# Kernel tuning notes

Hardware: AMD Instinct MI355X
Metric: run time of the kernel (lower is better)

The kernel has to match this reference:

```python
import jax, jax.numpy as jnp
import numpy as np

HEAD_DIM = 64


def setup_inputs() -> dict:
    key = jax.random.key(0)
    ks = jax.random.split(key, 5)
    B, T, D = 2, 2048, 1024
    x = jax.random.normal(ks[0], (B, T, D), dtype=jnp.float32)
    # Linear weights stored as [in, out]; scaled like typical init.
    w_qkv = jax.random.normal(ks[1], (D, 3 * D), dtype=jnp.float32) / np.sqrt(D)
    b_qkv = jax.random.normal(ks[2], (3 * D,), dtype=jnp.float32) * 0.02
    w_o = jax.random.normal(ks[3], (D, D), dtype=jnp.float32) / np.sqrt(D)
    b_o = jax.random.normal(ks[4], (D,), dtype=jnp.float32) * 0.02
    return {"x": x, "w_qkv": w_qkv, "b_qkv": b_qkv, "w_o": w_o, "b_o": b_o,
            "window": 256}


def reference(x, w_qkv, b_qkv, w_o, b_o, window):
    B, T, D = x.shape
    H = D // HEAD_DIM
    qkv = x @ w_qkv + b_qkv                      # [B, T, 3D]
    q, k, v = jnp.split(qkv, 3, axis=-1)
    # [B, H, T, hd]
    q = q.reshape(B, T, H, HEAD_DIM).transpose(0, 2, 1, 3)
    k = k.reshape(B, T, H, HEAD_DIM).transpose(0, 2, 1, 3)
    v = v.reshape(B, T, H, HEAD_DIM).transpose(0, 2, 1, 3)
    # Causal band mask: key j valid for query i iff 0 <= i - j <= window.
    idx = jnp.arange(T)
    diff = idx[:, None] - idx[None, :]
    mask = (diff >= 0) & (diff <= window)        # [T, T] bool
    scale = 1.0 / np.sqrt(HEAD_DIM)
    scores = jnp.einsum("bhqd,bhkd->bhqk", q, k) * scale
    scores = jnp.where(mask, scores, -jnp.inf)
    attn = jax.nn.softmax(scores, axis=-1)       # each row has >=1 valid entry
    out = jnp.einsum("bhqk,bhkd->bhqd", attn, v)  # [B, H, T, hd]
    out = out.transpose(0, 2, 1, 3).reshape(B, T, D)
    return out @ w_o + b_o
```

## Files before the change

### kernel.cpp

```cpp
#include <hip/hip_runtime.h>

#define T_SEQ 2048
#define DMODEL 1024
#define NH 16
#define HD 64

typedef unsigned short u16;
typedef short s16;
typedef __attribute__((ext_vector_type(8))) unsigned short u16x8;
typedef __attribute__((ext_vector_type(4))) unsigned short u16x4;
typedef __attribute__((ext_vector_type(8))) short bf16x8;
typedef __attribute__((ext_vector_type(4))) float f32x4;

__device__ __forceinline__ u16 f2bf(float f) {
    union { float f; unsigned u; } v; v.f = f;
    unsigned r = v.u + 0x7fffu + ((v.u >> 16) & 1u);
    return (u16)(r >> 16);
}
__device__ __forceinline__ float bf2f(u16 u) {
    union { unsigned u; float f; } v; v.u = ((unsigned)u) << 16;
    return v.f;
}

__device__ __forceinline__ void gl_lds16(const u16* g, u16* l) {
    __builtin_amdgcn_global_load_lds(
        (const __attribute__((address_space(1))) unsigned int*)g,
        (__attribute__((address_space(3))) unsigned int*)l, 16, 0, 0);
}

__global__ __launch_bounds__(256) void convert_kernel(
    const float* __restrict__ in, u16* __restrict__ out, int n)
{
    int idx = (blockIdx.x * 256 + threadIdx.x) * 4;
    if (idx < n) {
        float4 v = *reinterpret_cast<const float4*>(&in[idx]);
        u16x4 o;
        o.x = f2bf(v.x); o.y = f2bf(v.y); o.z = f2bf(v.z); o.w = f2bf(v.w);
        *reinterpret_cast<u16x4*>(&out[idx]) = o;
    }
}

__global__ __launch_bounds__(256) void transpose_convert_kernel(
    const float* __restrict__ in, u16* __restrict__ out, int K, int N)
{
    __shared__ u16 tile[64][65];
    const int tid = threadIdx.x;
    const int k0 = blockIdx.y * 64, n0 = blockIdx.x * 64;
    const int r  = tid >> 2;
    const int c4 = (tid & 3) * 16;
    #pragma unroll
    for (int i = 0; i < 4; ++i) {
        float4 v = *reinterpret_cast<const float4*>(&in[(size_t)(k0 + r) * N + n0 + c4 + i * 4]);
        tile[c4 + i*4 + 0][r] = f2bf(v.x);
        tile[c4 + i*4 + 1][r] = f2bf(v.y);
        tile[c4 + i*4 + 2][r] = f2bf(v.z);
        tile[c4 + i*4 + 3][r] = f2bf(v.w);
    }
    __syncthreads();
    u16x8 o0, o1;
    #pragma unroll
    for (int i = 0; i < 8; ++i) o0[i] = tile[r][c4 + i];
    #pragma unroll
    for (int i = 0; i < 8; ++i) o1[i] = tile[r][c4 + 8 + i];
    *reinterpret_cast<u16x8*>(&out[(size_t)(n0 + r) * K + k0 + c4])     = o0;
    *reinterpret_cast<u16x8*>(&out[(size_t)(n0 + r) * K + k0 + c4 + 8]) = o1;
}

template<int BM, int BN, bool OUT_BF16>
__global__ __launch_bounds__(256) void gemm_mfma_kernel(
    const u16* __restrict__ A, const u16* __restrict__ BT,
    const float* __restrict__ bias,
    float* __restrict__ C, u16* __restrict__ Cb,
    int M, int N, int K)
{
    constexpr int BK = 32;
    __shared__ __align__(16) u16 As[BM * BK];
    __shared__ __align__(16) u16 Bs[BN * BK];

    const int tid  = threadIdx.x;
    const int wave = tid >> 6, lane = tid & 63;
    const int m0 = blockIdx.y * BM, n0 = blockIdx.x * BN;

    constexpr int WM = BM / 2, WN = BN / 2;
    constexpr int MF = WM / 16, NF = WN / 16;
    const int wm = (wave >> 1) * WM, wn = (wave & 1) * WN;
    const int l15 = lane & 15, l4 = lane >> 4;

    f32x4 acc[MF][NF];
    #pragma unroll
    for (int nf = 0; nf < NF; ++nf) {
        const float bv = bias[n0 + wn + nf * 16 + l15];
        #pragma unroll
        for (int mf = 0; mf < MF; ++mf)
            acc[mf][nf] = (f32x4){bv, bv, bv, bv};
    }

    const int srow = tid >> 2;
    const int soff = (tid & 3) * 8;

    for (int k0 = 0; k0 < K; k0 += BK) {
        __syncthreads();
        gl_lds16(&A[(size_t)(m0 + srow) * K + k0 + soff],       &As[(size_t)tid * 8]);
        gl_lds16(&A[(size_t)(m0 + 64 + srow) * K + k0 + soff],  &As[(size_t)(tid + 256) * 8]);
        gl_lds16(&BT[(size_t)(n0 + srow) * K + k0 + soff],      &Bs[(size_t)tid * 8]);
        if constexpr (BN == 128)
            gl_lds16(&BT[(size_t)(n0 + 64 + srow) * K + k0 + soff], &Bs[(size_t)(tid + 256) * 8]);
        __syncthreads();

        bf16x8 af[MF], bf[NF];
        #pragma unroll
        for (int mf = 0; mf < MF; ++mf)
            af[mf] = *reinterpret_cast<const bf16x8*>(&As[(wm + mf * 16 + l15) * BK + l4 * 8]);
        #pragma unroll
        for (int nf = 0; nf < NF; ++nf)
            bf[nf] = *reinterpret_cast<const bf16x8*>(&Bs[(wn + nf * 16 + l15) * BK + l4 * 8]);
        #pragma unroll
        for (int mf = 0; mf < MF; ++mf)
            #pragma unroll
            for (int nf = 0; nf < NF; ++nf)
                acc[mf][nf] = __builtin_amdgcn_mfma_f32_16x16x32_bf16(af[mf], bf[nf], acc[mf][nf], 0, 0, 0);
    }

    #pragma unroll
    for (int mf = 0; mf < MF; ++mf)
        #pragma unroll
        for (int nf = 0; nf < NF; ++nf) {
            const int col = n0 + wn + nf * 16 + l15;
            #pragma unroll
            for (int r = 0; r < 4; ++r) {
                const int row = m0 + wm + mf * 16 + l4 * 4 + r;
                if constexpr (OUT_BF16) Cb[(size_t)row * N + col] = f2bf(acc[mf][nf][r]);
                else                    C [(size_t)row * N + col] = acc[mf][nf][r];
            }
        }
}

__global__ __launch_bounds__(256) void swa_mfma_kernel(
    const u16* __restrict__ qkv, u16* __restrict__ out,
    const int* __restrict__ wptr)
{
    const int window = *wptr;
    const int qt = blockIdx.x;
    const int bh = blockIdx.y;
    const int b  = bh >> 4;
    const int h  = bh & (NH - 1);

    const int tid  = threadIdx.x;
    const int wave = tid >> 6, lane = tid & 63;
    const int l15  = lane & 15, l4 = lane >> 4;
    const int hoff = h * HD;

    __shared__ __align__(16) s16 Ks[64 * 64];
    __shared__ __align__(16) s16 Vt[64 * 64];
    __shared__ __align__(16) s16 Ps[64 * 64];

    auto swz = [](int row, int col) { return (row * 64 + col) ^ ((row & 7) << 3); };

    const size_t qgrow = (size_t)(b * T_SEQ + qt * 64 + wave * 16 + l15) * (3 * DMODEL) + hoff;
    const bf16x8 qf0 = *reinterpret_cast<const bf16x8*>(&qkv[qgrow + l4 * 8]);
    const bf16x8 qf1 = *reinterpret_cast<const bf16x8*>(&qkv[qgrow + 32 + l4 * 8]);

    f32x4 oacc[4];
    #pragma unroll
    for (int nf = 0; nf < 4; ++nf) oacc[nf] = (f32x4){0.f, 0.f, 0.f, 0.f};
    float m[4] = {-1e30f, -1e30f, -1e30f, -1e30f};
    float l[4] = {0.f, 0.f, 0.f, 0.f};

    const int lo = qt * 64 - window;
    const int cstart = (lo <= 0) ? 0 : (lo >> 6);

    const int kr = tid >> 3;
    const int kc = (tid & 7) * 8;

    for (int c = cstart; c <= qt; ++c) {
        const int j0 = c * 64;
        __syncthreads();
        #pragma unroll
        for (int pass = 0; pass < 2; ++pass) {
            const int row = kr + pass * 32;
            const size_t g = (size_t)(b * T_SEQ + j0 + row) * (3 * DMODEL) + hoff + kc;
            const bf16x8 kv8 = *reinterpret_cast<const bf16x8*>(&qkv[g + DMODEL]);
            const bf16x8 vv8 = *reinterpret_cast<const bf16x8*>(&qkv[g + 2 * DMODEL]);
            *reinterpret_cast<bf16x8*>(&Ks[swz(row, kc)]) = kv8;
            #pragma unroll
            for (int i = 0; i < 8; ++i)
                Vt[swz(kc + i, row)] = vv8[i];
        }
        __syncthreads();

        f32x4 sacc[4];
        #pragma unroll
        for (int nf = 0; nf < 4; ++nf) sacc[nf] = (f32x4){0.f, 0.f, 0.f, 0.f};
        #pragma unroll
        for (int nf = 0; nf < 4; ++nf) {
            const bf16x8 kf0 = *reinterpret_cast<const bf16x8*>(&Ks[swz(nf * 16 + l15, l4 * 8)]);
            const bf16x8 kf1 = *reinterpret_cast<const bf16x8*>(&Ks[swz(nf * 16 + l15, 32 + l4 * 8)]);
            sacc[nf] = __builtin_amdgcn_mfma_f32_16x16x32_bf16(qf0, kf0, sacc[nf], 0, 0, 0);
            sacc[nf] = __builtin_amdgcn_mfma_f32_16x16x32_bf16(qf1, kf1, sacc[nf], 0, 0, 0);
        }

        float p[4][4];
        #pragma unroll
        for (int r = 0; r < 4; ++r) {
            const int iq = qt * 64 + wave * 16 + l4 * 4 + r;
            float rmax = -1e30f;
            #pragma unroll
            for (int nf = 0; nf < 4; ++nf) {
                const int diff = iq - (j0 + nf * 16 + l15);
                const bool valid = (diff >= 0) && (diff <= window);
                const float s = valid ? sacc[nf][r] * 0.125f : -1e30f;
                p[r][nf] = s;
                rmax = fmaxf(rmax, s);
            }
            rmax = fmaxf(rmax, __shfl_xor(rmax, 1));
            rmax = fmaxf(rmax, __shfl_xor(rmax, 2));
            rmax = fmaxf(rmax, __shfl_xor(rmax, 4));
            rmax = fmaxf(rmax, __shfl_xor(rmax, 8));
            const float mn = fmaxf(m[r], rmax);
            const float rf = __expf(m[r] - mn);
            float rs = 0.f;
            #pragma unroll
            for (int nf = 0; nf < 4; ++nf) {
                const float e = __expf(p[r][nf] - mn);
                p[r][nf] = e;
                rs += e;
            }
            rs += __shfl_xor(rs, 1);
            rs += __shfl_xor(rs, 2);
            rs += __shfl_xor(rs, 4);
            rs += __shfl_xor(rs, 8);
            l[r] = l[r] * rf + rs;
            m[r] = mn;
            #pragma unroll
            for (int nf = 0; nf < 4; ++nf) oacc[nf][r] *= rf;
            #pragma unroll
            for (int nf = 0; nf < 4; ++nf)
                Ps[swz(wave * 16 + l4 * 4 + r, nf * 16 + l15)] = (s16)f2bf(p[r][nf]);
        }
        __syncthreads();

        #pragma unroll
        for (int ks = 0; ks < 2; ++ks) {
            const bf16x8 pa = *reinterpret_cast<const bf16x8*>(&Ps[swz(wave * 16 + l15, ks * 32 + l4 * 8)]);
            #pragma unroll
            for (int nf = 0; nf < 4; ++nf) {
                const bf16x8 vf = *reinterpret_cast<const bf16x8*>(&Vt[swz(nf * 16 + l15, ks * 32 + l4 * 8)]);
                oacc[nf] = __builtin_amdgcn_mfma_f32_16x16x32_bf16(pa, vf, oacc[nf], 0, 0, 0);
            }
        }
    }

    #pragma unroll
    for (int r = 0; r < 4; ++r) {
        const float inv = 1.f / l[r];
        const size_t orow = (size_t)(b * T_SEQ + qt * 64 + wave * 16 + l4 * 4 + r) * DMODEL + hoff;
        #pragma unroll
        for (int nf = 0; nf < 4; ++nf)
            out[orow + nf * 16 + l15] = f2bf(oacc[nf][r] * inv);
    }
}

extern "C" void kernel_launch(void* const* d_in, const int* in_sizes, int n_in,
                              void* d_out, int out_size, void* d_ws, size_t ws_size,
                              hipStream_t stream) {
    (void)in_sizes; (void)n_in; (void)out_size; (void)ws_size;

    const float* x     = (const float*)d_in[0];
    const float* w_qkv = (const float*)d_in[1];
    const float* b_qkv = (const float*)d_in[2];
    const float* w_o   = (const float*)d_in[3];
    const float* b_o   = (const float*)d_in[4];
    const int*   wnd   = (const int*)d_in[5];

    const int M = 2 * T_SEQ;

    char* w = (char*)d_ws;
    u16* qkvb  = (u16*)(w);
    u16* attb  = (u16*)(w + 24u * 1024 * 1024);
    u16* xb    = (u16*)(w + 32u * 1024 * 1024);
    u16* wqkvT = (u16*)(w + 40u * 1024 * 1024);
    u16* woT   = (u16*)(w + 46u * 1024 * 1024);

    dim3 blk(256);

    convert_kernel<<<dim3((M * DMODEL / 4 + 255) / 256), blk, 0, stream>>>(x, xb, M * DMODEL);
    transpose_convert_kernel<<<dim3(3 * DMODEL / 64, DMODEL / 64), blk, 0, stream>>>(
        w_qkv, wqkvT, DMODEL, 3 * DMODEL);
    transpose_convert_kernel<<<dim3(DMODEL / 64, DMODEL / 64), blk, 0, stream>>>(
        w_o, woT, DMODEL, DMODEL);

    gemm_mfma_kernel<128, 128, true><<<dim3(3 * DMODEL / 128, M / 128), blk, 0, stream>>>(
        xb, wqkvT, b_qkv, nullptr, qkvb, M, 3 * DMODEL, DMODEL);

    swa_mfma_kernel<<<dim3(T_SEQ / 64, 2 * NH), blk, 0, stream>>>(qkvb, attb, wnd);

    gemm_mfma_kernel<128, 64, false><<<dim3(DMODEL / 64, M / 128), blk, 0, stream>>>(
        attb, woT, b_o, (float*)d_out, nullptr, M, DMODEL, DMODEL);
}
```

Baseline: 176.6 us.

## Double GEMM K-tile to 64 with XOR-swizzled LDS and fix V-transpose bank conflicts

The GEMM K tile grows from 32 to 64, which halves the number of barrier-separated load/compute iterations. Global-to-LDS loads are placed with an XOR swizzle on the 8-element column chunk so the fragment reads avoid bank conflicts. The attention kernel's transposed V buffer gets a new swizzle function so the scalar transposed writes and the vector reads conflict less. The cost is doubled LDS per GEMM block, which can lower occupancy, and more fragment registers.

New measurement: 165.3 us. -6.4%, faster.

```diff
diff --git a/kernel.cpp b/kernel.cpp
--- a/kernel.cpp
+++ b/kernel.cpp
@@ -16,10 +16,6 @@
     union { float f; unsigned u; } v; v.f = f;
     unsigned r = v.u + 0x7fffu + ((v.u >> 16) & 1u);
     return (u16)(r >> 16);
-}
-__device__ __forceinline__ float bf2f(u16 u) {
-    union { unsigned u; float f; } v; v.u = ((unsigned)u) << 16;
-    return v.f;
 }
 
 __device__ __forceinline__ void gl_lds16(const u16* g, u16* l) {
@@ -73,7 +69,7 @@
     float* __restrict__ C, u16* __restrict__ Cb,
     int M, int N, int K)
 {
-    constexpr int BK = 32;
+    constexpr int BK = 64;
     __shared__ __align__(16) u16 As[BM * BK];
     __shared__ __align__(16) u16 Bs[BN * BK];
 
@@ -85,6 +81,7 @@
     constexpr int MF = WM / 16, NF = WN / 16;
     const int wm = (wave >> 1) * WM, wn = (wave & 1) * WN;
     const int l15 = lane & 15, l4 = lane >> 4;
+    const int l7  = l15 & 7;
 
     f32x4 acc[MF][NF];
     #pragma unroll
@@ -95,30 +92,47 @@
             acc[mf][nf] = (f32x4){bv, bv, bv, bv};
     }
 
-    const int srow = tid >> 2;
-    const int soff = (tid & 3) * 8;
+    constexpr int ALOADS = BM / 32;
+    constexpr int BLOADS = BN / 32;
 
     for (int k0 = 0; k0 < K; k0 += BK) {
         __syncthreads();
-        gl_lds16(&A[(size_t)(m0 + srow) * K + k0 + soff],       &As[(size_t)tid * 8]);
-        gl_lds16(&A[(size_t)(m0 + 64 + srow) * K + k0 + soff],  &As[(size_t)(tid + 256) * 8]);
-        gl_lds16(&BT[(size_t)(n0 + srow) * K + k0 + soff],      &Bs[(size_t)tid * 8]);
-        if constexpr (BN == 128)
-            gl_lds16(&BT[(size_t)(n0 + 64 + srow) * K + k0 + soff], &Bs[(size_t)(tid + 256) * 8]);
-        __syncthreads();
-
-        bf16x8 af[MF], bf[NF];
-        #pragma unroll
-        for (int mf = 0; mf < MF; ++mf)
-            af[mf] = *reinterpret_cast<const bf16x8*>(&As[(wm + mf * 16 + l15) * BK + l4 * 8]);
-        #pragma unroll
-        for (int nf = 0; nf < NF; ++nf)
-            bf[nf] = *reinterpret_cast<const bf16x8*>(&Bs[(wn + nf * 16 + l15) * BK + l4 * 8]);
-        #pragma unroll
-        for (int mf = 0; mf < MF; ++mf)
+        #pragma unroll
+        for (int i = 0; i < ALOADS; ++i) {
+            const int p = tid + i * 256;
+            const int r = p >> 3, c = p & 7;
+            gl_lds16(&A[(size_t)(m0 + r) * K + k0 + ((c ^ (r & 7)) * 8)], &As[(size_t)p * 8]);
+        }
+        #pragma unroll
+        for (int i = 0; i < BLOADS; ++i) {
+            const int p = tid + i * 256;
+            const int r = p >> 3, c = p & 7;
+            gl_lds16(&BT[(size_t)(n0 + r) * K + k0 + ((c ^ (r & 7)) * 8)], &Bs[(size_t)p * 8]);
+        }
+        __syncthreads();
+
+        bf16x8 af[MF][2], bfr[NF][2];
+        #pragma unroll
+        for (int kk = 0; kk < 2; ++kk) {
+            const int cc = kk * 4 + l4;
+            const int cs = cc ^ l7;
+            #pragma unroll
+            for (int mf = 0; mf < MF; ++mf)
+                af[mf][kk] = *reinterpret_cast<const bf16x8*>(
+                    &As[(size_t)((wm + mf * 16 + l15) * 8 + cs) * 8]);
             #pragma unroll
             for (int nf = 0; nf < NF; ++nf)
-                acc[mf][nf] = __builtin_amdgcn_mfma_f32_16x16x32_bf16(af[mf], bf[nf], acc[mf][nf], 0, 0, 0);
+                bfr[nf][kk] = *reinterpret_cast<const bf16x8*>(
+                    &Bs[(size_t)((wn + nf * 16 + l15) * 8 + cs) * 8]);
+        }
+        #pragma unroll
+        for (int kk = 0; kk < 2; ++kk)
+            #pragma unroll
+            for (int mf = 0; mf < MF; ++mf)
+                #pragma unroll
+                for (int nf = 0; nf < NF; ++nf)
+                    acc[mf][nf] = __builtin_amdgcn_mfma_f32_16x16x32_bf16(
+                        af[mf][kk], bfr[nf][kk], acc[mf][nf], 0, 0, 0);
     }
 
     #pragma unroll
@@ -155,6 +169,7 @@
     __shared__ __align__(16) s16 Ps[64 * 64];
 
     auto swz = [](int row, int col) { return (row * 64 + col) ^ ((row & 7) << 3); };
+    auto vtx = [](int d, int k) { return d * 64 + (((k >> 3) ^ (d >> 3)) & 7) * 8 + (k & 7); };
 
     const size_t qgrow = (size_t)(b * T_SEQ + qt * 64 + wave * 16 + l15) * (3 * DMODEL) + hoff;
     const bf16x8 qf0 = *reinterpret_cast<const bf16x8*>(&qkv[qgrow + l4 * 8]);
@@ -184,7 +199,7 @@
             *reinterpret_cast<bf16x8*>(&Ks[swz(row, kc)]) = kv8;
             #pragma unroll
             for (int i = 0; i < 8; ++i)
-                Vt[swz(kc + i, row)] = vv8[i];
+                Vt[vtx(kc + i, row)] = vv8[i];
         }
         __syncthreads();
 
@@ -244,7 +259,7 @@
             const bf16x8 pa = *reinterpret_cast<const bf16x8*>(&Ps[swz(wave * 16 + l15, ks * 32 + l4 * 8)]);
             #pragma unroll
             for (int nf = 0; nf < 4; ++nf) {
-                const bf16x8 vf = *reinterpret_cast<const bf16x8*>(&Vt[swz(nf * 16 + l15, ks * 32 + l4 * 8)]);
+                const bf16x8 vf = *reinterpret_cast<const bf16x8*>(&Vt[vtx(nf * 16 + l15, ks * 32 + l4 * 8)]);
                 oacc[nf] = __builtin_amdgcn_mfma_f32_16x16x32_bf16(pa, vf, oacc[nf], 0, 0, 0);
             }
         }
@@ -283,7 +298,7 @@
 
     dim3 blk(256);
 
-    convert_kernel<<<dim3((M * DMODEL / 4 + 255) / 256), blk, 0, stream>>>(x, xb, M * DMODEL);
+    convert_kernel<<<dim3(M * DMODEL / 4 / 256), blk, 0, stream>>>(x, xb, M * DMODEL);
     transpose_convert_kernel<<<dim3(3 * DMODEL / 64, DMODEL / 64), blk, 0, stream>>>(
         w_qkv, wqkvT, DMODEL, 3 * DMODEL);
     transpose_convert_kernel<<<dim3(DMODEL / 64, DMODEL / 64), blk, 0, stream>>>(
```
